# Kernel optimization log

Measured on AMD Instinct MI355X. Metric: run time of the kernel, lower is better.

The kernel has to match this reference:

```python
import jax, jax.numpy as jnp
import numpy as np

D, H, FFN, SEG, L, RCL, T, B = 1024, 16, 4096, 128, 32, 4, 2048, 2
N = T // SEG          # 16 segments
M = N - 1             # 15 memory frames (training-mode Emformer convention)
R = RCL * N           # 64 right-context frames
S = N                 # summary length from AvgPool1d(kernel=stride=SEG, ceil_mode)
Q = R + T + S         # 2128 query rows
KV = M + R + T        # 2127 key rows
NEG_INF = -1e8
EPS = 1e-5

def _layer_norm(x, g, b):
    m = jnp.mean(x, axis=-1, keepdims=True)
    v = jnp.mean((x - m) ** 2, axis=-1, keepdims=True)
    return (x - m) * jax.lax.rsqrt(v + EPS) * g + b

def _make_attention_mask():
    # True = disallowed. Per-segment Emformer banding: each segment attends to
    # prior memory slots, its own right-context block, and left-context + own segment.
    mask = np.ones((Q, KV), dtype=bool)
    for i in range(N):
        cols = np.zeros(KV, dtype=bool)
        cols[max(0, i - M):i] = True                                   # memory bank
        cols[M + i * RCL: M + (i + 1) * RCL] = True                    # own right ctx
        cols[M + R + max(0, i * SEG - L): M + R + (i + 1) * SEG] = True  # left ctx + segment
        allowed = ~cols
        mask[i * RCL:(i + 1) * RCL] = allowed        # right-context query rows
        mask[R + i * SEG: R + (i + 1) * SEG] = allowed  # utterance query rows
        mask[R + T + i] = allowed                    # summary query row
    return jnp.asarray(mask)

def setup_inputs() -> dict:
    key = jax.random.key(0)
    ks = jax.random.split(key, 10)
    w = lambda k, s: 0.02 * jax.random.normal(k, s, jnp.float32)
    return {
        "utterance": jax.random.normal(ks[0], (T, B, D), jnp.float32),
        "right_context": jax.random.normal(ks[1], (R, B, D), jnp.float32),
        "mems": jax.random.normal(ks[2], (M, B, D), jnp.float32),
        "ln_in_g": jnp.ones((D,), jnp.float32), "ln_in_b": jnp.zeros((D,), jnp.float32),
        "Wq": w(ks[3], (D, D)), "bq": jnp.zeros((D,), jnp.float32),
        "Wkv": w(ks[4], (2 * D, D)), "bkv": jnp.zeros((2 * D,), jnp.float32),
        "Wo": w(ks[5], (D, D)), "bo": jnp.zeros((D,), jnp.float32),
        "ff_ln_g": jnp.ones((D,), jnp.float32), "ff_ln_b": jnp.zeros((D,), jnp.float32),
        "W1": w(ks[6], (FFN, D)), "b1": jnp.zeros((FFN,), jnp.float32),
        "W2": w(ks[7], (D, FFN)), "b2": jnp.zeros((D,), jnp.float32),
        "ln_out_g": jnp.ones((D,), jnp.float32), "ln_out_b": jnp.zeros((D,), jnp.float32),
        "lengths": jnp.full((B,), T, jnp.int32),
        "attention_mask": _make_attention_mask(),
    }

def reference(utterance, right_context, mems, ln_in_g, ln_in_b, Wq, bq, Wkv, bkv, Wo, bo,
              ff_ln_g, ff_ln_b, W1, b1, W2, b2, ln_out_g, ln_out_b, lengths, attention_mask):
    dh = D // H
    scaling = dh ** -0.5
    # Pre-attention layer norm over concat([right_context, utterance])
    ln = _layer_norm(jnp.concatenate([right_context, utterance], axis=0), ln_in_g, ln_in_b)
    ln_rc, ln_utt = ln[:R], ln[R:]
    # AvgPool1d(kernel=stride=SEG) summary over time (T divisible by SEG)
    summary = ln_utt.reshape(N, SEG, B, D).mean(axis=1)                # (S,B,D)
    query = jnp.concatenate([ln_rc, ln_utt, summary], axis=0) @ Wq.T + bq   # (Q,B,D)
    kv = jnp.concatenate([mems, ln_rc, ln_utt], axis=0) @ Wkv.T + bkv       # (KV,B,2D)
    k_all, v_all = kv[..., :D], kv[..., D:]
    heads = lambda t: t.reshape(t.shape[0], B * H, dh).transpose(1, 0, 2)   # (B*H,L,dh)
    q, k, v = heads(query) * scaling, heads(k_all), heads(v_all)
    aw = jnp.einsum('bqd,bkd->bqk', q, k)                               # (B*H,Q,KV)
    aw = jnp.where(attention_mask[None], NEG_INF, aw)
    # padding mask over key axis: klengths = lengths + M + (R + T - max(lengths))
    klengths = lengths + M + R + T - jnp.max(lengths)
    padding_mask = jnp.arange(KV)[None, :] >= klengths[:, None]         # (B,KV)
    aw = aw.reshape(B, H, Q, KV)
    aw = jnp.where(padding_mask[:, None, None, :], NEG_INF, aw).reshape(B * H, Q, KV)
    probs = jax.nn.softmax(aw, axis=-1)
    attn = jnp.einsum('bqk,bkd->bqd', probs, v).transpose(1, 0, 2).reshape(Q, B, D)
    out = attn @ Wo.T + bo
    rc_output = out[:R + T]
    out_mems = jnp.clip(out[R + T:], -10.0, 10.0)                       # tanh_on_mem=False
    # Residual + pos-FF + output layer norm
    result = rc_output + jnp.concatenate([right_context, utterance], axis=0)
    ff = _layer_norm(result, ff_ln_g, ff_ln_b)
    ff = jax.nn.relu(ff @ W1.T + b1) @ W2.T + b2
    result = _layer_norm(result + ff, ln_out_g, ln_out_b)
    return result[R:], result[:R], out_mems
```

## Files before the change

### kernel.cpp

```cpp
#include <hip/hip_runtime.h>

constexpr int D   = 1024;
constexpr int H   = 16;
constexpr int FFN = 4096;
constexpr int SEG = 128;
constexpr int L   = 32;
constexpr int RCL = 4;
constexpr int T   = 2048;
constexpr int B   = 2;
constexpr int N   = T / SEG;
constexpr int M   = N - 1;
constexpr int R   = RCL * N;
constexpr int Q   = R + T + N;
constexpr int KV  = M + R + T;
constexpr int RT  = R + T;
constexpr float EPS = 1e-5f;
constexpr int MPAD = 4352;

typedef float f32x4 __attribute__((ext_vector_type(4)));
typedef __bf16 bf16x8 __attribute__((ext_vector_type(8)));
typedef short s16x4 __attribute__((ext_vector_type(4)));

__device__ __forceinline__ ushort bf16rne(float x) {
    unsigned u = __float_as_uint(x);
    return (ushort)((u + 0x7FFFu + ((u >> 16) & 1u)) >> 16);
}
__device__ __forceinline__ float bf2f(ushort h) {
    return __uint_as_float(((unsigned)h) << 16);
}

__device__ inline void block_reduce_2(float& s1, float& s2) {
    #pragma unroll
    for (int off = 32; off > 0; off >>= 1) {
        s1 += __shfl_xor(s1, off, 64);
        s2 += __shfl_xor(s2, off, 64);
    }
    __shared__ float red[8];
    int lane = threadIdx.x & 63, w = threadIdx.x >> 6;
    if (lane == 0) { red[w * 2] = s1; red[w * 2 + 1] = s2; }
    __syncthreads();
    s1 = red[0] + red[2] + red[4] + red[6];
    s2 = red[1] + red[3] + red[5] + red[7];
}

__device__ __forceinline__ void gload16(const void* g, void* l) {
    __builtin_amdgcn_global_load_lds(
        (__attribute__((address_space(1))) void*)(uintptr_t)g,
        (__attribute__((address_space(3))) void*)(unsigned)(uintptr_t)l,
        16, 0, 0);
}

__global__ __launch_bounds__(256) void zpad_kernel(ushort* __restrict__ Bp, int n4) {
    int idx = blockIdx.x * 256 + threadIdx.x;
    if (idx < n4) {
        s16x4 z = {0, 0, 0, 0};
        *reinterpret_cast<s16x4*>(&Bp[(size_t)idx * 4]) = z;
    }
}

__global__ __launch_bounds__(256) void ln2_kernel(const float* __restrict__ src0,
                                                  const float* __restrict__ src1,
                                                  int split,
                                                  float* __restrict__ dstF, int remap,
                                                  ushort* __restrict__ B0,
                                                  ushort* __restrict__ B1,
                                                  int rowoff1,
                                                  const float* __restrict__ gamma,
                                                  const float* __restrict__ beta) {
    int row = blockIdx.x;
    int t = threadIdx.x;
    const float* src = (row < split) ? src0 + (size_t)row * D
                                     : src1 + (size_t)(row - split) * D;
    float4 x = *reinterpret_cast<const float4*>(&src[t * 4]);
    float s1 = x.x + x.y + x.z + x.w;
    float s2 = x.x * x.x + x.y * x.y + x.z * x.z + x.w * x.w;
    block_reduce_2(s1, s2);
    float mean = s1 * (1.0f / D);
    float var  = s2 * (1.0f / D) - mean * mean;
    float rs = rsqrtf(var + EPS);
    float4 g4 = *reinterpret_cast<const float4*>(&gamma[t * 4]);
    float4 b4 = *reinterpret_cast<const float4*>(&beta[t * 4]);
    float y[4];
    y[0] = (x.x - mean) * rs * g4.x + b4.x;
    y[1] = (x.y - mean) * rs * g4.y + b4.y;
    y[2] = (x.z - mean) * rs * g4.z + b4.z;
    y[3] = (x.w - mean) * rs * g4.w + b4.w;
    if (dstF) {
        size_t off;
        if (!remap) off = (size_t)row * D;
        else off = (row < R * B) ? ((size_t)T * B * D + (size_t)row * D)
                                 : ((size_t)(row - R * B) * D);
        *reinterpret_cast<float4*>(&dstF[off + t * 4]) =
            make_float4(y[0], y[1], y[2], y[3]);
    }
    if (B0) {
        s16x4 h4;
        #pragma unroll
        for (int j = 0; j < 4; ++j) h4[j] = (short)bf16rne(y[j]);
        size_t o0 = (size_t)row * D + t * 4;
        *reinterpret_cast<s16x4*>(&B0[o0]) = h4;
        if (B1) {
            size_t o1 = (size_t)(row + rowoff1) * D + t * 4;
            *reinterpret_cast<s16x4*>(&B1[o1]) = h4;
        }
    }
}

__global__ __launch_bounds__(256) void summary3_kernel(const float* __restrict__ qxF,
                                                       ushort* __restrict__ qxB) {
    int nb = blockIdx.x;
    int n = nb >> 1, b = nb & 1;
    int t = threadIdx.x;
    float acc[4] = {0.f, 0.f, 0.f, 0.f};
    for (int s = 0; s < SEG; ++s) {
        size_t base = ((size_t)((R + n * SEG + s) * B + b)) * D + t * 4;
        float4 x = *reinterpret_cast<const float4*>(&qxF[base]);
        acc[0] += x.x; acc[1] += x.y; acc[2] += x.z; acc[3] += x.w;
    }
    s16x4 h4;
    #pragma unroll
    for (int j = 0; j < 4; ++j) h4[j] = (short)bf16rne(acc[j] * (1.0f / SEG));
    size_t dst = ((size_t)(RT * B + nb)) * D + t * 4;
    *reinterpret_cast<s16x4*>(&qxB[dst]) = h4;
}

__global__ __launch_bounds__(256) void cvt_bf16(const float* __restrict__ src,
                                                ushort* __restrict__ dst,
                                                int Mr, int kshift, int n4) {
    int idx = blockIdx.x * 256 + threadIdx.x;
    if (idx >= n4) return;
    int row = idx >> kshift;
    size_t e = (size_t)idx * 4;
    s16x4 h = {0, 0, 0, 0};
    if (row < Mr) {
        float4 x = *reinterpret_cast<const float4*>(&src[e]);
        h[0] = (short)bf16rne(x.x);
        h[1] = (short)bf16rne(x.y);
        h[2] = (short)bf16rne(x.z);
        h[3] = (short)bf16rne(x.w);
    }
    *reinterpret_cast<s16x4*>(&dst[e]) = h;
}

__global__ __launch_bounds__(256) void gemm_bf(const ushort* __restrict__ A,
                                               const ushort* __restrict__ W,
                                               const float* __restrict__ bias,
                                               const float* __restrict__ residual,
                                               float* __restrict__ C,
                                               ushort* __restrict__ CB,
                                               int Mr, int Nc, int Kd,
                                               float alpha, int do_relu, int gx) {
    __shared__ __align__(16) ushort sm[2 * 4096];
    ushort* sA = sm;
    ushort* sW = sm + 4096;

    int bid = blockIdx.x;
    int nwg = gridDim.x;
    int q8 = nwg >> 3, r8 = nwg & 7;
    int c8 = bid & 7, j8 = bid >> 3;
    int lin = (c8 < r8 ? c8 * (q8 + 1) : r8 * (q8 + 1) + (c8 - r8) * q8) + j8;
    const int bn0 = (lin % gx) * 128;
    const int bm0 = (lin / gx) * 128;

    const int t = threadIdx.x;
    const int w = t >> 6, lane = t & 63;
    const int wr = w >> 1, wc = w & 1;
    const int fr = lane & 15, fq = lane >> 4;

    const int srow = lane >> 2;
    const int scol = (lane & 3) * 8;
    const size_t aR0 = (size_t)(bm0 + w * 32 + srow) * Kd + scol;
    const size_t aR1 = aR0 + (size_t)16 * Kd;
    const size_t wR0 = (size_t)(bn0 + w * 32 + srow) * Kd + scol;
    const size_t wR1 = wR0 + (size_t)16 * Kd;
    const int lbase = w * 1024;

    f32x4 acc[4][4];
    #pragma unroll
    for (int m = 0; m < 4; ++m)
        #pragma unroll
        for (int n = 0; n < 4; ++n) acc[m][n] = f32x4{0.f, 0.f, 0.f, 0.f};

    const int ao = (wr * 64 + fr) * 32 + fq * 8;
    const int wo = (wc * 64 + fr) * 32 + fq * 8;

    for (int k0 = 0; k0 < Kd; k0 += 32) {
        gload16(A + aR0 + k0, sA + lbase);
        gload16(A + aR1 + k0, sA + lbase + 512);
        gload16(W + wR0 + k0, sW + lbase);
        gload16(W + wR1 + k0, sW + lbase + 512);
        __syncthreads();

        bf16x8 bh[4];
        #pragma unroll
        for (int n = 0; n < 4; ++n)
            bh[n] = *reinterpret_cast<const bf16x8*>(&sW[wo + n * 512]);
        #pragma unroll
        for (int m = 0; m < 4; ++m) {
            bf16x8 ah = *reinterpret_cast<const bf16x8*>(&sA[ao + m * 512]);
            #pragma unroll
            for (int n = 0; n < 4; ++n)
                acc[m][n] = __builtin_amdgcn_mfma_f32_16x16x32_bf16(ah, bh[n], acc[m][n], 0, 0, 0);
        }
        __syncthreads();
    }

    float bv[4];
    #pragma unroll
    for (int n = 0; n < 4; ++n) bv[n] = bias[bn0 + wc * 64 + n * 16 + fr];
    #pragma unroll
    for (int m = 0; m < 4; ++m) {
        #pragma unroll
        for (int j = 0; j < 4; ++j) {
            int row = bm0 + wr * 64 + m * 16 + fq * 4 + j;
            if (row < Mr) {
                #pragma unroll
                for (int n = 0; n < 4; ++n) {
                    int col = bn0 + wc * 64 + n * 16 + fr;
                    float v = (acc[m][n][j] + bv[n]) * alpha;
                    if (do_relu) v = fmaxf(v, 0.f);
                    if (residual) v += residual[(size_t)row * Nc + col];
                    if (CB) CB[(size_t)row * Nc + col] = bf16rne(v);
                    else    C[(size_t)row * Nc + col] = v;
                }
            }
        }
    }
}

constexpr int KTS = 181;
constexpr int CST = 186;
constexpr int CMX = 192;

__global__ __launch_bounds__(256) void attn2(const float* __restrict__ qb,
                                             const float* __restrict__ kb,
                                             const float* __restrict__ vb,
                                             const int* __restrict__ lengths,
                                             ushort* __restrict__ outB) {
    __shared__ __align__(16) float  Kt[64 * KTS];
    __shared__ __align__(16) ushort Vt[64 * CST];
    __shared__ __align__(16) float  ps[4][2][CMX];
    __shared__ __align__(16) float  qs[4][2][64];
    __shared__ int colmap[CMX];

    int gid = blockIdx.x;
    int half = gid & 1;
    int i = (gid >> 1) & 15;
    int h = (gid >> 5) & 15;
    int b = gid >> 9;
    int t = threadIdx.x;
    int lane = t & 63, w = t >> 6;

    int nm = i;
    int u0 = (i * SEG - L > 0) ? (i * SEG - L) : 0;
    int nc = nm + RCL + (i + 1) * SEG - u0;

    int maxlen = max(lengths[0], lengths[1]);
    int kl = lengths[b] + (M + R + T) - maxlen;

    for (int c = t; c < nc; c += 256) {
        int g;
        if (c < nm)            g = c;
        else if (c < nm + RCL) g = M + i * RCL + (c - nm);
        else                   g = M + R + u0 + (c - nm - RCL);
        colmap[c] = g;
    }
    __syncthreads();

    for (int f = t; f < nc * 16; f += 256) {
        int c = f >> 4, dc = f & 15;
        int g = colmap[c];
        size_t base = ((size_t)g * B + b) * D + h * 64 + dc * 4;
        float4 k4 = *reinterpret_cast<const float4*>(&kb[base]);
        Kt[(dc * 4 + 0) * KTS + c] = k4.x;
        Kt[(dc * 4 + 1) * KTS + c] = k4.y;
        Kt[(dc * 4 + 2) * KTS + c] = k4.z;
        Kt[(dc * 4 + 3) * KTS + c] = k4.w;
        float4 v4 = *reinterpret_cast<const float4*>(&vb[base]);
        Vt[(dc * 4 + 0) * CST + c] = bf16rne(v4.x);
        Vt[(dc * 4 + 1) * CST + c] = bf16rne(v4.y);
        Vt[(dc * 4 + 2) * CST + c] = bf16rne(v4.z);
        Vt[(dc * 4 + 3) * CST + c] = bf16rne(v4.w);
    }
    __syncthreads();

    const int nrows = half ? 65 : 68;
    const int rbase = half ? 68 : 0;
    const int c0 = lane, c1 = lane + 64, c2 = lane + 128;
    bool v0 = (c0 < nc) && (colmap[c0] < kl);
    bool v1 = (c1 < nc) && (colmap[c1] < kl);
    bool v2 = (c2 < nc) && (colmap[c2] < kl);

    for (int rl = w * 2; rl < nrows; rl += 8) {
        int r0 = rbase + rl;
        bool two = (rl + 1 < nrows);
        int r1 = two ? r0 + 1 : r0;
        int qrow0 = (r0 < RCL) ? i * RCL + r0
                  : (r0 < 132) ? R + i * SEG + (r0 - RCL)
                               : R + T + i;
        int qrow1 = (r1 < RCL) ? i * RCL + r1
                  : (r1 < 132) ? R + i * SEG + (r1 - RCL)
                               : R + T + i;

        qs[w][0][lane] = qb[((size_t)qrow0 * B + b) * D + h * 64 + lane];
        qs[w][1][lane] = qb[((size_t)qrow1 * B + b) * D + h * 64 + lane];
        asm volatile("" ::: "memory");

        float a00 = 0.f, a01 = 0.f, a02 = 0.f;
        float a10 = 0.f, a11 = 0.f, a12 = 0.f;
        #pragma unroll
        for (int d = 0; d < 64; d += 4) {
            float4 q0 = *reinterpret_cast<const float4*>(&qs[w][0][d]);
            float4 q1 = *reinterpret_cast<const float4*>(&qs[w][1][d]);
            #pragma unroll
            for (int dd = 0; dd < 4; ++dd) {
                float k0 = Kt[(d + dd) * KTS + c0];
                float k1 = Kt[(d + dd) * KTS + c1];
                float k2 = Kt[(d + dd) * KTS + c2];
                float qa = (dd == 0) ? q0.x : (dd == 1) ? q0.y : (dd == 2) ? q0.z : q0.w;
                float qbv = (dd == 0) ? q1.x : (dd == 1) ? q1.y : (dd == 2) ? q1.z : q1.w;
                a00 += qa * k0;  a01 += qa * k1;  a02 += qa * k2;
                a10 += qbv * k0; a11 += qbv * k1; a12 += qbv * k2;
            }
        }
        float s00 = v0 ? a00 : -1e30f, s01 = v1 ? a01 : -1e30f, s02 = v2 ? a02 : -1e30f;
        float s10 = v0 ? a10 : -1e30f, s11 = v1 ? a11 : -1e30f, s12 = v2 ? a12 : -1e30f;

        float m0 = fmaxf(fmaxf(s00, s01), s02);
        float m1 = fmaxf(fmaxf(s10, s11), s12);
        #pragma unroll
        for (int off = 32; off > 0; off >>= 1) {
            m0 = fmaxf(m0, __shfl_xor(m0, off, 64));
            m1 = fmaxf(m1, __shfl_xor(m1, off, 64));
        }
        float p00 = __expf(s00 - m0), p01 = __expf(s01 - m0), p02 = __expf(s02 - m0);
        float p10 = __expf(s10 - m1), p11 = __expf(s11 - m1), p12 = __expf(s12 - m1);
        float sum0 = p00 + p01 + p02, sum1 = p10 + p11 + p12;
        #pragma unroll
        for (int off = 32; off > 0; off >>= 1) {
            sum0 += __shfl_xor(sum0, off, 64);
            sum1 += __shfl_xor(sum1, off, 64);
        }
        ps[w][0][c0] = p00; ps[w][0][c1] = p01; ps[w][0][c2] = p02;
        ps[w][1][c0] = p10; ps[w][1][c1] = p11; ps[w][1][c2] = p12;
        asm volatile("" ::: "memory");

        float o0 = 0.f, o1 = 0.f;
        const ushort* vrow = &Vt[lane * CST];
        int c = 0;
        for (; c + 4 <= nc; c += 4) {
            float4 pv0 = *reinterpret_cast<const float4*>(&ps[w][0][c]);
            float4 pv1 = *reinterpret_cast<const float4*>(&ps[w][1][c]);
            unsigned va = *reinterpret_cast<const unsigned*>(&vrow[c]);
            unsigned vb2 = *reinterpret_cast<const unsigned*>(&vrow[c + 2]);
            float vf0 = __uint_as_float(va << 16);
            float vf1 = __uint_as_float(va & 0xFFFF0000u);
            float vf2 = __uint_as_float(vb2 << 16);
            float vf3 = __uint_as_float(vb2 & 0xFFFF0000u);
            o0 += pv0.x * vf0 + pv0.y * vf1 + pv0.z * vf2 + pv0.w * vf3;
            o1 += pv1.x * vf0 + pv1.y * vf1 + pv1.z * vf2 + pv1.w * vf3;
        }
        for (; c < nc; ++c) {
            float vf = bf2f(vrow[c]);
            o0 += ps[w][0][c] * vf;
            o1 += ps[w][1][c] * vf;
        }

        size_t ob0 = ((size_t)qrow0 * B + b) * D + h * 64 + lane;
        outB[ob0] = bf16rne(o0 / sum0);
        if (two) {
            size_t ob1 = ((size_t)qrow1 * B + b) * D + h * 64 + lane;
            outB[ob1] = bf16rne(o1 / sum1);
        }
    }
}

__global__ __launch_bounds__(256) void resid_clip(const float* __restrict__ obuf,
                                                  const float* __restrict__ rc,
                                                  const float* __restrict__ utt,
                                                  float* __restrict__ result,
                                                  float* __restrict__ out_mems) {
    size_t idx = (size_t)blockIdx.x * 256 + threadIdx.x;
    size_t f = idx * 4;
    if (f >= (size_t)Q * B * D) return;
    int row = (int)(f >> 10);
    float4 o = *reinterpret_cast<const float4*>(&obuf[f]);
    if (row < RT * B) {
        const float* res = (row < R * B) ? &rc[f] : &utt[f - (size_t)R * B * D];
        float4 rv = *reinterpret_cast<const float4*>(res);
        o.x += rv.x; o.y += rv.y; o.z += rv.z; o.w += rv.w;
        *reinterpret_cast<float4*>(&result[f]) = o;
    } else {
        o.x = fminf(fmaxf(o.x, -10.f), 10.f);
        o.y = fminf(fmaxf(o.y, -10.f), 10.f);
        o.z = fminf(fmaxf(o.z, -10.f), 10.f);
        o.w = fminf(fmaxf(o.w, -10.f), 10.f);
        *reinterpret_cast<float4*>(&out_mems[f - (size_t)RT * B * D]) = o;
    }
}

extern "C" void kernel_launch(void* const* d_in, const int* in_sizes, int n_in,
                              void* d_out, int out_size, void* d_ws, size_t ws_size,
                              hipStream_t stream) {
    const float* utt   = (const float*)d_in[0];
    const float* rc    = (const float*)d_in[1];
    const float* mems  = (const float*)d_in[2];
    const float* lng   = (const float*)d_in[3];
    const float* lnb   = (const float*)d_in[4];
    const float* Wq    = (const float*)d_in[5];
    const float* bq    = (const float*)d_in[6];
    const float* Wkv   = (const float*)d_in[7];
    const float* bkv   = (const float*)d_in[8];
    const float* Wo    = (const float*)d_in[9];
    const float* bo    = (const float*)d_in[10];
    const float* ffg   = (const float*)d_in[11];
    const float* ffb   = (const float*)d_in[12];
    const float* W1    = (const float*)d_in[13];
    const float* b1    = (const float*)d_in[14];
    const float* W2    = (const float*)d_in[15];
    const float* b2    = (const float*)d_in[16];
    const float* outg  = (const float*)d_in[17];
    const float* outb  = (const float*)d_in[18];
    const int*   lens  = (const int*)d_in[19];

    constexpr int QBD  = Q * B * D;
    constexpr int KVBD = KV * B * D;

    float* ws = (float*)d_ws;
    size_t off = 0;
    auto allocF = [&](size_t n) { float* p = ws + off; off += (n + 63) & ~(size_t)63; return p; };
    auto allocU = [&](size_t n) { ushort* p = (ushort*)(ws + off); off += ((n + 1) / 2 + 63) & ~(size_t)63; return p; };

    float* f_q  = allocF(QBD);
    float* f_k  = allocF(KVBD);
    float* f_v  = allocF(KVBD);
    float* qxF  = allocF((size_t)RT * B * D);
    ushort* qxB = allocU((size_t)MPAD * D);
    ushort* kvB = allocU((size_t)MPAD * D);
    ushort* atB = allocU((size_t)MPAD * D);
    ushort* flB = allocU((size_t)RT * B * D);
    ushort* fhB = allocU((size_t)RT * B * FFN);
    ushort* wB  = allocU((size_t)FFN * D);
    float* obuf   = f_q;
    float* result = f_v;
    float* res2   = f_k;
    float* out = (float*)d_out;

    auto wconv = [&](const float* src, int Mr, int Kd) {
        int kshift = (Kd == 1024) ? 8 : 10;
        int n4 = Mr * (Kd >> 2);
        cvt_bf16<<<(n4 + 255) / 256, 256, 0, stream>>>(src, wB, Mr, kshift, n4);
    };
    auto gemm = [&](const ushort* a, const float* bias, const float* resid,
                    float* C, ushort* CB,
                    int Mr, int Mpad, int Nc, int Kd, float alpha, int relu) {
        int gx = Nc / 128, gy = Mpad / 128;
        gemm_bf<<<gx * gy, 256, 0, stream>>>(a, wB, bias, resid, C, CB,
                                             Mr, Nc, Kd, alpha, relu, gx);
    };

    zpad_kernel<<<96, 256, 0, stream>>>(qxB + (size_t)Q * B * D, (MPAD - Q * B) * D / 4);
    zpad_kernel<<<98, 256, 0, stream>>>(kvB + (size_t)KV * B * D, (MPAD - KV * B) * D / 4);
    zpad_kernel<<<96, 256, 0, stream>>>(atB + (size_t)Q * B * D, (MPAD - Q * B) * D / 4);
    cvt_bf16<<<(M * B * 256 + 255) / 256, 256, 0, stream>>>(mems, kvB, M * B, 8,
                                                            M * B * 256);
    ln2_kernel<<<RT * B, 256, 0, stream>>>(rc, utt, R * B, qxF, 0,
                                           qxB, kvB, M * B, lng, lnb);
    summary3_kernel<<<N * B, 256, 0, stream>>>(qxF, qxB);
    wconv(Wq, D, D);
    gemm(qxB, bq, nullptr, f_q, nullptr, Q * B, MPAD, D, D, 0.125f, 0);
    wconv(Wkv, D, D);
    gemm(kvB, bkv, nullptr, f_k, nullptr, KV * B, MPAD, D, D, 1.0f, 0);
    wconv(Wkv + (size_t)D * D, D, D);
    gemm(kvB, bkv + D, nullptr, f_v, nullptr, KV * B, MPAD, D, D, 1.0f, 0);
    attn2<<<N * B * H * 2, 256, 0, stream>>>(f_q, f_k, f_v, lens, atB);
    wconv(Wo, D, D);
    gemm(atB, bo, nullptr, obuf, nullptr, Q * B, MPAD, D, D, 1.0f, 0);
    resid_clip<<<(Q * B * D / 4 + 255) / 256, 256, 0, stream>>>(
        obuf, rc, utt, result, out + (size_t)(T + R) * B * D);
    ln2_kernel<<<RT * B, 256, 0, stream>>>(result, result, RT * B, nullptr, 0,
                                           flB, nullptr, 0, ffg, ffb);
    wconv(W1, FFN, D);
    gemm(flB, b1, nullptr, nullptr, fhB, RT * B, RT * B, FFN, D, 1.0f, 1);
    wconv(W2, D, FFN);
    gemm(fhB, b2, result, res2, nullptr, RT * B, RT * B, D, FFN, 1.0f, 0);
    ln2_kernel<<<RT * B, 256, 0, stream>>>(res2, res2, RT * B, out, 1,
                                           nullptr, nullptr, 0, outg, outb);
}
```

Before: 654.6 us.

## Batch weight conversions into one prep kernel, fuse K/V GEMM, fp16 dot2 attention

Merges all weight bf16 conversions, mems conversion and pad zeroing into a single prep kernel. K and V projections become one GEMM with a 2048-wide output, so the attention kernel reads K and V from one interleaved buffer. The attention kernel is rewritten to store K, V, Q and probabilities as fp16 in swizzled LDS and to compute dot products with fdot2, handling four query rows per wave instead of two. This cuts launch count and LDS use and raises ALU throughput, but drops the score and probability arithmetic to fp16 precision.

```diff
diff --git a/kernel.cpp b/kernel.cpp
--- a/kernel.cpp
+++ b/kernel.cpp
@@ -16,18 +16,27 @@
 constexpr int RT  = R + T;
 constexpr float EPS = 1e-5f;
 constexpr int MPAD = 4352;
+constexpr int KVSTR = 2048;
 
 typedef float f32x4 __attribute__((ext_vector_type(4)));
 typedef __bf16 bf16x8 __attribute__((ext_vector_type(8)));
 typedef short s16x4 __attribute__((ext_vector_type(4)));
+typedef unsigned u32x4 __attribute__((ext_vector_type(4)));
+typedef ushort us4 __attribute__((ext_vector_type(4)));
+typedef _Float16 h2_t __attribute__((ext_vector_type(2)));
 
 __device__ __forceinline__ ushort bf16rne(float x) {
     unsigned u = __float_as_uint(x);
     return (ushort)((u + 0x7FFFu + ((u >> 16) & 1u)) >> 16);
 }
-__device__ __forceinline__ float bf2f(ushort h) {
-    return __uint_as_float(((unsigned)h) << 16);
-}
+__device__ __forceinline__ ushort f2h(float x) {
+    _Float16 h = (_Float16)x;
+    ushort u; __builtin_memcpy(&u, &h, 2); return u;
+}
+__device__ __forceinline__ h2_t uh2(unsigned u) {
+    h2_t h; __builtin_memcpy(&h, &u, 4); return h;
+}
+#define FDOT2(a, b, c) __builtin_amdgcn_fdot2((a), (b), (c), false)
 
 __device__ inline void block_reduce_2(float& s1, float& s2) {
     #pragma unroll
@@ -50,12 +59,44 @@
         16, 0, 0);
 }
 
-__global__ __launch_bounds__(256) void zpad_kernel(ushort* __restrict__ Bp, int n4) {
+__global__ __launch_bounds__(256) void prep_kernel(const float* __restrict__ Wq,
+                                                   const float* __restrict__ Wkv,
+                                                   const float* __restrict__ Wo,
+                                                   const float* __restrict__ W1,
+                                                   const float* __restrict__ W2,
+                                                   const float* __restrict__ mems,
+                                                   ushort* __restrict__ wAll,
+                                                   ushort* __restrict__ kvB,
+                                                   ushort* __restrict__ qxB,
+                                                   ushort* __restrict__ atB) {
     int idx = blockIdx.x * 256 + threadIdx.x;
-    if (idx < n4) {
-        s16x4 z = {0, 0, 0, 0};
-        *reinterpret_cast<s16x4*>(&Bp[(size_t)idx * 4]) = z;
-    }
+    constexpr int n0 = D * D / 4;
+    constexpr int n1 = n0 + 2 * D * D / 4;
+    constexpr int n2 = n1 + D * D / 4;
+    constexpr int n3 = n2 + FFN * D / 4;
+    constexpr int n4 = n3 + FFN * D / 4;
+    constexpr int n5 = n4 + M * B * D / 4;
+    constexpr int n6 = n5 + (MPAD - Q * B) * D / 4;
+    constexpr int n7 = n6 + (MPAD - KV * B) * D / 4;
+    constexpr int n8 = n7 + (MPAD - Q * B) * D / 4;
+    if (idx >= n8) return;
+    const float* src = nullptr; ushort* dst; int rel;
+    if (idx < n0)      { src = Wq;   dst = wAll;                              rel = idx; }
+    else if (idx < n1) { src = Wkv;  dst = wAll + D * D;                      rel = idx - n0; }
+    else if (idx < n2) { src = Wo;   dst = wAll + 3 * D * D;                  rel = idx - n1; }
+    else if (idx < n3) { src = W1;   dst = wAll + 4 * D * D;                  rel = idx - n2; }
+    else if (idx < n4) { src = W2;   dst = wAll + 4 * D * D + FFN * D;        rel = idx - n3; }
+    else if (idx < n5) { src = mems; dst = kvB;                               rel = idx - n4; }
+    else if (idx < n6) { dst = qxB + (size_t)Q * B * D;                       rel = idx - n5; }
+    else if (idx < n7) { dst = kvB + (size_t)KV * B * D;                      rel = idx - n6; }
+    else               { dst = atB + (size_t)Q * B * D;                       rel = idx - n7; }
+    s16x4 hv = {0, 0, 0, 0};
+    if (src) {
+        float4 x = *reinterpret_cast<const float4*>(&src[(size_t)rel * 4]);
+        hv[0] = (short)bf16rne(x.x); hv[1] = (short)bf16rne(x.y);
+        hv[2] = (short)bf16rne(x.z); hv[3] = (short)bf16rne(x.w);
+    }
+    *reinterpret_cast<s16x4*>(&dst[(size_t)rel * 4]) = hv;
 }
 
 __global__ __launch_bounds__(256) void ln2_kernel(const float* __restrict__ src0,
@@ -124,24 +165,6 @@
     *reinterpret_cast<s16x4*>(&qxB[dst]) = h4;
 }
 
-__global__ __launch_bounds__(256) void cvt_bf16(const float* __restrict__ src,
-                                                ushort* __restrict__ dst,
-                                                int Mr, int kshift, int n4) {
-    int idx = blockIdx.x * 256 + threadIdx.x;
-    if (idx >= n4) return;
-    int row = idx >> kshift;
-    size_t e = (size_t)idx * 4;
-    s16x4 h = {0, 0, 0, 0};
-    if (row < Mr) {
-        float4 x = *reinterpret_cast<const float4*>(&src[e]);
-        h[0] = (short)bf16rne(x.x);
-        h[1] = (short)bf16rne(x.y);
-        h[2] = (short)bf16rne(x.z);
-        h[3] = (short)bf16rne(x.w);
-    }
-    *reinterpret_cast<s16x4*>(&dst[e]) = h;
-}
-
 __global__ __launch_bounds__(256) void gemm_bf(const ushort* __restrict__ A,
                                                const ushort* __restrict__ W,
                                                const float* __restrict__ bias,
@@ -228,19 +251,16 @@
     }
 }
 
-constexpr int KTS = 181;
-constexpr int CST = 186;
 constexpr int CMX = 192;
 
-__global__ __launch_bounds__(256) void attn2(const float* __restrict__ qb,
-                                             const float* __restrict__ kb,
-                                             const float* __restrict__ vb,
+__global__ __launch_bounds__(256) void attn4(const float* __restrict__ qb,
+                                             const float* __restrict__ kvbuf,
                                              const int* __restrict__ lengths,
                                              ushort* __restrict__ outB) {
-    __shared__ __align__(16) float  Kt[64 * KTS];
-    __shared__ __align__(16) ushort Vt[64 * CST];
-    __shared__ __align__(16) float  ps[4][2][CMX];
-    __shared__ __align__(16) float  qs[4][2][64];
+    __shared__ __align__(16) ushort K2[CMX * 64];
+    __shared__ __align__(16) ushort Vt[64 * CMX];
+    __shared__ __align__(16) ushort ps[4][4][CMX];
+    __shared__ __align__(16) ushort qs[4][4][64];
     __shared__ int colmap[CMX];
 
     int gid = blockIdx.x;
@@ -254,6 +274,7 @@
     int nm = i;
     int u0 = (i * SEG - L > 0) ? (i * SEG - L) : 0;
     int nc = nm + RCL + (i + 1) * SEG - u0;
+    int nc4 = (nc + 7) & ~7;
 
     int maxlen = max(lengths[0], lengths[1]);
     int kl = lengths[b] + (M + R + T) - maxlen;
@@ -270,17 +291,21 @@
     for (int f = t; f < nc * 16; f += 256) {
         int c = f >> 4, dc = f & 15;
         int g = colmap[c];
-        size_t base = ((size_t)g * B + b) * D + h * 64 + dc * 4;
-        float4 k4 = *reinterpret_cast<const float4*>(&kb[base]);
-        Kt[(dc * 4 + 0) * KTS + c] = k4.x;
-        Kt[(dc * 4 + 1) * KTS + c] = k4.y;
-        Kt[(dc * 4 + 2) * KTS + c] = k4.z;
-        Kt[(dc * 4 + 3) * KTS + c] = k4.w;
-        float4 v4 = *reinterpret_cast<const float4*>(&vb[base]);
-        Vt[(dc * 4 + 0) * CST + c] = bf16rne(v4.x);
-        Vt[(dc * 4 + 1) * CST + c] = bf16rne(v4.y);
-        Vt[(dc * 4 + 2) * CST + c] = bf16rne(v4.z);
-        Vt[(dc * 4 + 3) * CST + c] = bf16rne(v4.w);
+        size_t base = ((size_t)g * B + b) * KVSTR + h * 64 + dc * 4;
+        float4 k4 = *reinterpret_cast<const float4*>(&kvbuf[base]);
+        float4 v4 = *reinterpret_cast<const float4*>(&kvbuf[base + 1024]);
+        us4 kh = {(ushort)f2h(k4.x), (ushort)f2h(k4.y), (ushort)f2h(k4.z), (ushort)f2h(k4.w)};
+        *reinterpret_cast<us4*>((char*)K2 + c * 128 + ((dc * 8) ^ ((c & 7) << 4))) = kh;
+        int d0 = dc * 4;
+        *(ushort*)((char*)Vt + (d0 + 0) * 384 + ((c * 2) ^ (((d0 + 0) & 7) << 4))) = f2h(v4.x);
+        *(ushort*)((char*)Vt + (d0 + 1) * 384 + ((c * 2) ^ (((d0 + 1) & 7) << 4))) = f2h(v4.y);
+        *(ushort*)((char*)Vt + (d0 + 2) * 384 + ((c * 2) ^ (((d0 + 2) & 7) << 4))) = f2h(v4.z);
+        *(ushort*)((char*)Vt + (d0 + 3) * 384 + ((c * 2) ^ (((d0 + 3) & 7) << 4))) = f2h(v4.w);
+    }
+    for (int f = t; f < 512; f += 256) {
+        int c = nc + (f & 7), d = f >> 3;
+        if (c < nc4)
+            *(ushort*)((char*)Vt + d * 384 + ((c * 2) ^ ((d & 7) << 4))) = 0;
     }
     __syncthreads();
 
@@ -290,87 +315,101 @@
     bool v0 = (c0 < nc) && (colmap[c0] < kl);
     bool v1 = (c1 < nc) && (colmap[c1] < kl);
     bool v2 = (c2 < nc) && (colmap[c2] < kl);
-
-    for (int rl = w * 2; rl < nrows; rl += 8) {
-        int r0 = rbase + rl;
-        bool two = (rl + 1 < nrows);
-        int r1 = two ? r0 + 1 : r0;
-        int qrow0 = (r0 < RCL) ? i * RCL + r0
-                  : (r0 < 132) ? R + i * SEG + (r0 - RCL)
-                               : R + T + i;
-        int qrow1 = (r1 < RCL) ? i * RCL + r1
-                  : (r1 < 132) ? R + i * SEG + (r1 - RCL)
-                               : R + T + i;
-
-        qs[w][0][lane] = qb[((size_t)qrow0 * B + b) * D + h * 64 + lane];
-        qs[w][1][lane] = qb[((size_t)qrow1 * B + b) * D + h * 64 + lane];
+    const int xm0 = (c0 & 7) << 4, xm1 = (c1 & 7) << 4, xm2 = (c2 & 7) << 4;
+
+    for (int rl = w * 4; rl < nrows; rl += 16) {
+        int qrow[4]; bool rv[4];
+        #pragma unroll
+        for (int j = 0; j < 4; ++j) {
+            int r = rl + j;
+            rv[j] = (r < nrows);
+            int rr = rbase + (rv[j] ? r : rl);
+            qrow[j] = (rr < RCL) ? i * RCL + rr
+                    : (rr < 132) ? R + i * SEG + (rr - RCL)
+                                 : R + T + i;
+        }
+        #pragma unroll
+        for (int j = 0; j < 4; ++j)
+            qs[w][j][lane] = f2h(qb[((size_t)qrow[j] * B + b) * D + h * 64 + lane]);
         asm volatile("" ::: "memory");
 
-        float a00 = 0.f, a01 = 0.f, a02 = 0.f;
-        float a10 = 0.f, a11 = 0.f, a12 = 0.f;
-        #pragma unroll
-        for (int d = 0; d < 64; d += 4) {
-            float4 q0 = *reinterpret_cast<const float4*>(&qs[w][0][d]);
-            float4 q1 = *reinterpret_cast<const float4*>(&qs[w][1][d]);
+        float a[4][3];
+        #pragma unroll
+        for (int r = 0; r < 4; ++r) { a[r][0] = 0.f; a[r][1] = 0.f; a[r][2] = 0.f; }
+
+        #pragma unroll
+        for (int j8 = 0; j8 < 8; ++j8) {
+            u32x4 kk0 = *reinterpret_cast<const u32x4*>((char*)K2 + c0 * 128 + ((j8 * 16) ^ xm0));
+            u32x4 kk1 = *reinterpret_cast<const u32x4*>((char*)K2 + c1 * 128 + ((j8 * 16) ^ xm1));
+            u32x4 kk2 = *reinterpret_cast<const u32x4*>((char*)K2 + c2 * 128 + ((j8 * 16) ^ xm2));
             #pragma unroll
-            for (int dd = 0; dd < 4; ++dd) {
-                float k0 = Kt[(d + dd) * KTS + c0];
-                float k1 = Kt[(d + dd) * KTS + c1];
-                float k2 = Kt[(d + dd) * KTS + c2];
-                float qa = (dd == 0) ? q0.x : (dd == 1) ? q0.y : (dd == 2) ? q0.z : q0.w;
-                float qbv = (dd == 0) ? q1.x : (dd == 1) ? q1.y : (dd == 2) ? q1.z : q1.w;
-                a00 += qa * k0;  a01 += qa * k1;  a02 += qa * k2;
-                a10 += qbv * k0; a11 += qbv * k1; a12 += qbv * k2;
+            for (int r = 0; r < 4; ++r) {
+                u32x4 qq = *reinterpret_cast<const u32x4*>(&qs[w][r][j8 * 8]);
+                #pragma unroll
+                for (int e = 0; e < 4; ++e) {
+                    a[r][0] = FDOT2(uh2(qq[e]), uh2(kk0[e]), a[r][0]);
+                    a[r][1] = FDOT2(uh2(qq[e]), uh2(kk1[e]), a[r][1]);
+                    a[r][2] = FDOT2(uh2(qq[e]), uh2(kk2[e]), a[r][2]);
+                }
             }
         }
-        float s00 = v0 ? a00 : -1e30f, s01 = v1 ? a01 : -1e30f, s02 = v2 ? a02 : -1e30f;
-        float s10 = v0 ? a10 : -1e30f, s11 = v1 ? a11 : -1e30f, s12 = v2 ? a12 : -1e30f;
-
-        float m0 = fmaxf(fmaxf(s00, s01), s02);
-        float m1 = fmaxf(fmaxf(s10, s11), s12);
+
+        float p[4][3], mrow[4], sum[4];
+        #pragma unroll
+        for (int r = 0; r < 4; ++r) {
+            float s0 = v0 ? a[r][0] : -1e30f;
+            float s1 = v1 ? a[r][1] : -1e30f;
+            float s2 = v2 ? a[r][2] : -1e30f;
+            a[r][0] = s0; a[r][1] = s1; a[r][2] = s2;
+            mrow[r] = fmaxf(fmaxf(s0, s1), s2);
+        }
         #pragma unroll
         for (int off = 32; off > 0; off >>= 1) {
-            m0 = fmaxf(m0, __shfl_xor(m0, off, 64));
-            m1 = fmaxf(m1, __shfl_xor(m1, off, 64));
-        }
-        float p00 = __expf(s00 - m0), p01 = __expf(s01 - m0), p02 = __expf(s02 - m0);
-        float p10 = __expf(s10 - m1), p11 = __expf(s11 - m1), p12 = __expf(s12 - m1);
-        float sum0 = p00 + p01 + p02, sum1 = p10 + p11 + p12;
+            #pragma unroll
+            for (int r = 0; r < 4; ++r)
+                mrow[r] = fmaxf(mrow[r], __shfl_xor(mrow[r], off, 64));
+        }
+        #pragma unroll
+        for (int r = 0; r < 4; ++r) {
+            p[r][0] = __expf(a[r][0] - mrow[r]);
+            p[r][1] = __expf(a[r][1] - mrow[r]);
+            p[r][2] = __expf(a[r][2] - mrow[r]);
+            sum[r] = p[r][0] + p[r][1] + p[r][2];
+        }
         #pragma unroll
         for (int off = 32; off > 0; off >>= 1) {
-            sum0 += __shfl_xor(sum0, off, 64);
-            sum1 += __shfl_xor(sum1, off, 64);
-        }
-        ps[w][0][c0] = p00; ps[w][0][c1] = p01; ps[w][0][c2] = p02;
-        ps[w][1][c0] = p10; ps[w][1][c1] = p11; ps[w][1][c2] = p12;
+            #pragma unroll
+            for (int r = 0; r < 4; ++r)
+                sum[r] += __shfl_xor(sum[r], off, 64);
+        }
+        #pragma unroll
+        for (int r = 0; r < 4; ++r) {
+            ps[w][r][c0] = f2h(p[r][0]);
+            ps[w][r][c1] = f2h(p[r][1]);
+            ps[w][r][c2] = f2h(p[r][2]);
+        }
         asm volatile("" ::: "memory");
 
-        float o0 = 0.f, o1 = 0.f;
-        const ushort* vrow = &Vt[lane * CST];
-        int c = 0;
-        for (; c + 4 <= nc; c += 4) {
-            float4 pv0 = *reinterpret_cast<const float4*>(&ps[w][0][c]);
-            float4 pv1 = *reinterpret_cast<const float4*>(&ps[w][1][c]);
-            unsigned va = *reinterpret_cast<const unsigned*>(&vrow[c]);
-            unsigned vb2 = *reinterpret_cast<const unsigned*>(&vrow[c + 2]);
-            float vf0 = __uint_as_float(va << 16);
-            float vf1 = __uint_as_float(va & 0xFFFF0000u);
-            float vf2 = __uint_as_float(vb2 << 16);
-            float vf3 = __uint_as_float(vb2 & 0xFFFF0000u);
-            o0 += pv0.x * vf0 + pv0.y * vf1 + pv0.z * vf2 + pv0.w * vf3;
-            o1 += pv1.x * vf0 + pv1.y * vf1 + pv1.z * vf2 + pv1.w * vf3;
-        }
-        for (; c < nc; ++c) {
-            float vf = bf2f(vrow[c]);
-            o0 += ps[w][0][c] * vf;
-            o1 += ps[w][1][c] * vf;
-        }
-
-        size_t ob0 = ((size_t)qrow0 * B + b) * D + h * 64 + lane;
-        outB[ob0] = bf16rne(o0 / sum0);
-        if (two) {
-            size_t ob1 = ((size_t)qrow1 * B + b) * D + h * 64 + lane;
-            outB[ob1] = bf16rne(o1 / sum1);
+        float o[4] = {0.f, 0.f, 0.f, 0.f};
+        const char* vrow = (const char*)Vt + lane * 384;
+        const int xmv = (lane & 7) << 4;
+        for (int c = 0; c < nc4; c += 8) {
+            u32x4 vv = *reinterpret_cast<const u32x4*>(vrow + ((c * 2) ^ xmv));
+            #pragma unroll
+            for (int r = 0; r < 4; ++r) {
+                u32x4 pp = *reinterpret_cast<const u32x4*>(&ps[w][r][c]);
+                o[r] = FDOT2(uh2(pp[0]), uh2(vv[0]), o[r]);
+                o[r] = FDOT2(uh2(pp[1]), uh2(vv[1]), o[r]);
+                o[r] = FDOT2(uh2(pp[2]), uh2(vv[2]), o[r]);
+                o[r] = FDOT2(uh2(pp[3]), uh2(vv[3]), o[r]);
+            }
+        }
+        #pragma unroll
+        for (int r = 0; r < 4; ++r) {
+            if (rv[r]) {
+                size_t ob = ((size_t)qrow[r] * B + b) * D + h * 64 + lane;
+                outB[ob] = bf16rne(o[r] / sum[r]);
+            }
         }
     }
 }
@@ -431,59 +470,53 @@
     auto allocF = [&](size_t n) { float* p = ws + off; off += (n + 63) & ~(size_t)63; return p; };
     auto allocU = [&](size_t n) { ushort* p = (ushort*)(ws + off); off += ((n + 1) / 2 + 63) & ~(size_t)63; return p; };
 
-    float* f_q  = allocF(QBD);
-    float* f_k  = allocF(KVBD);
-    float* f_v  = allocF(KVBD);
-    float* qxF  = allocF((size_t)RT * B * D);
-    ushort* qxB = allocU((size_t)MPAD * D);
-    ushort* kvB = allocU((size_t)MPAD * D);
-    ushort* atB = allocU((size_t)MPAD * D);
-    ushort* flB = allocU((size_t)RT * B * D);
-    ushort* fhB = allocU((size_t)RT * B * FFN);
-    ushort* wB  = allocU((size_t)FFN * D);
+    float* f_q   = allocF(QBD);
+    float* f_kv  = allocF((size_t)KVBD * 2);
+    float* qxF   = allocF((size_t)RT * B * D);
+    ushort* qxB  = allocU((size_t)MPAD * D);
+    ushort* kvB  = allocU((size_t)MPAD * D);
+    ushort* atB  = allocU((size_t)MPAD * D);
+    ushort* flB  = allocU((size_t)RT * B * D);
+    ushort* fhB  = allocU((size_t)RT * B * FFN);
+    ushort* wAll = allocU((size_t)4 * D * D + 2 * (size_t)FFN * D);
     float* obuf   = f_q;
-    float* result = f_v;
-    float* res2   = f_k;
+    float* result = f_kv;
+    float* res2   = f_kv + (size_t)RT * B * D;
     float* out = (float*)d_out;
 
-    auto wconv = [&](const float* src, int Mr, int Kd) {
-        int kshift = (Kd == 1024) ? 8 : 10;
-        int n4 = Mr * (Kd >> 2);
-        cvt_bf16<<<(n4 + 255) / 256, 256, 0, stream>>>(src, wB, Mr, kshift, n4);
-    };
-    auto gemm = [&](const ushort* a, const float* bias, const float* resid,
-                    float* C, ushort* CB,
+    const ushort* wq  = wAll;
+    const ushort* wkv = wAll + (size_t)D * D;
+    const ushort* wo  = wAll + (size_t)3 * D * D;
+    const ushort* w1  = wAll + (size_t)4 * D * D;
+    const ushort* w2  = wAll + (size_t)4 * D * D + (size_t)FFN * D;
+
+    auto gemm = [&](const ushort* a, const ushort* wgt, const float* bias,
+                    const float* resid, float* C, ushort* CB,
                     int Mr, int Mpad, int Nc, int Kd, float alpha, int relu) {
         int gx = Nc / 128, gy = Mpad / 128;
-        gemm_bf<<<gx * gy, 256, 0, stream>>>(a, wB, bias, resid, C, CB,
+        gemm_bf<<<gx * gy, 256, 0, stream>>>(a, wgt, bias, resid, C, CB,
                                              Mr, Nc, Kd, alpha, relu, gx);
     };
 
-    zpad_kernel<<<96, 256, 0, stream>>>(qxB + (size_t)Q * B * D, (MPAD - Q * B) * D / 4);
-    zpad_kernel<<<98, 256, 0, stream>>>(kvB + (size_t)KV * B * D, (MPAD - KV * B) * D / 4);
-    zpad_kernel<<<96, 256, 0, stream>>>(atB + (size_t)Q * B * D, (MPAD - Q * B) * D / 4);
-    cvt_bf16<<<(M * B * 256 + 255) / 256, 256, 0, stream>>>(mems, kvB, M * B, 8,
-                                                            M * B * 256);
+    {
+        constexpr int n8 = 4 * D * D / 4 + 2 * FFN * D / 4 + M * B * D / 4
+                         + 2 * (MPAD - Q * B) * D / 4 + (MPAD - KV * B) * D / 4;
+        prep_kernel<<<(n8 + 255) / 256, 256, 0, stream>>>(Wq, Wkv, Wo, W1, W2, mems,
+                                                          wAll, kvB, qxB, atB);
+    }
     ln2_kernel<<<RT * B, 256, 0, stream>>>(rc, utt, R * B, qxF, 0,
                                            qxB, kvB, M * B, lng, lnb);
     summary3_kernel<<<N * B, 256, 0, stream>>>(qxF, qxB);
-    wconv(Wq, D, D);
-    gemm(qxB, bq, nullptr, f_q, nullptr, Q * B, MPAD, D, D, 0.125f, 0);
-    wconv(Wkv, D, D);
-    gemm(kvB, bkv, nullptr, f_k, nullptr, KV * B, MPAD, D, D, 1.0f, 0);
-    wconv(Wkv + (size_t)D * D, D, D);
-    gemm(kvB, bkv + D, nullptr, f_v, nullptr, KV * B, MPAD, D, D, 1.0f, 0);
-    attn2<<<N * B * H * 2, 256, 0, stream>>>(f_q, f_k, f_v, lens, atB);
-    wconv(Wo, D, D);
-    gemm(atB, bo, nullptr, obuf, nullptr, Q * B, MPAD, D, D, 1.0f, 0);
+    gemm(qxB, wq, bq, nullptr, f_q, nullptr, Q * B, MPAD, D, D, 0.125f, 0);
+    gemm(kvB, wkv, bkv, nullptr, f_kv, nullptr, KV * B, MPAD, KVSTR, D, 1.0f, 0);
+    attn4<<<N * B * H * 2, 256, 0, stream>>>(f_q, f_kv, lens, atB);
+    gemm(atB, wo, bo, nullptr, obuf, nullptr, Q * B, MPAD, D, D, 1.0f, 0);
     resid_clip<<<(Q * B * D / 4 + 255) / 256, 256, 0, stream>>>(
         obuf, rc, utt, result, out + (size_t)(T + R) * B * D);
     ln2_kernel<<<RT * B, 256, 0, stream>>>(result, result, RT * B, nullptr, 0,
                                            flB, nullptr, 0, ffg, ffb);
-    wconv(W1, FFN, D);
-    gemm(flB, b1, nullptr, nullptr, fhB, RT * B, RT * B, FFN, D, 1.0f, 1);
-    wconv(W2, D, FFN);
-    gemm(fhB, b2, result, res2, nullptr, RT * B, RT * B, D, FFN, 1.0f, 0);
+    gemm(flB, w1, b1, nullptr, nullptr, fhB, RT * B, RT * B, FFN, D, 1.0f, 1);
+    gemm(fhB, w2, b2, result, res2, nullptr, RT * B, RT * B, D, FFN, 1.0f, 0);
     ln2_kernel<<<RT * B, 256, 0, stream>>>(res2, res2, RT * B, out, 1,
                                            nullptr, nullptr, 0, outg, outb);
 }
```

Measured after the change: 584.0 us. 1.12x faster.
